# Kernel tuning notes

Hardware: AMD Instinct MI355X
Metric: run time of the kernel (lower is better)

Reference implementation:

```python
import jax, jax.numpy as jnp
import numpy as np
from jax import lax

VOL = 96 ** 3        # AvgPool3d(kernel_size=96) pooling volume
GAMMA = 0.2          # cam_threshold (gamma default in update())
NUM_CLASSES = 14


def conv3d_same(x, w, b):
    # Conv3d(kernel_size=3, padding=1), NCDHW layout
    y = lax.conv_general_dilated(
        x, w, window_strides=(1, 1, 1),
        padding=((1, 1), (1, 1), (1, 1)),
        dimension_numbers=('NCDHW', 'OIDHW', 'NCDHW'))
    return y + b[None, :, None, None, None]


def maxpool3d_2(x):
    return lax.reduce_window(x, -jnp.inf, lax.max,
                             (1, 1, 2, 2, 2), (1, 1, 2, 2, 2), 'VALID')


def dom_classifier(x, c1w, c1b, c2w, c2b, lw, lb):
    x = jax.nn.relu(maxpool3d_2(conv3d_same(x, c1w, c1b)))   # [N,128,2,2,2]
    x = jax.nn.relu(maxpool3d_2(conv3d_same(x, c2w, c2b)))   # [N,64,1,1,1]
    x = x.reshape(x.shape[0], -1)                            # [N,64]
    return x @ lw.T + lb                                     # [N,1]


def get_cam(feature):
    # torch.autograd.functional.jacobian of AvgPool3d(96) on a [1,C,96,96,96]
    # input is analytically delta(c,c')/96^3 at every voxel; the subsequent
    # mean over spatial dims keeps eye(C)/96^3. Same math, closed form.
    n, c = feature.shape[:2]
    weight = jnp.broadcast_to(jnp.eye(c, dtype=feature.dtype) / VOL, (n, c, c))
    # einsum(weight, feature, 'n cls ch, n ch h w d -> n cls h w d')
    cam = jnp.einsum('nkc,ncxyz->nkxyz', weight, feature)
    return jax.nn.relu(cam)


def reference(feature, masks, dom_feat, conv1_w, conv1_b, conv2_w, conv2_b,
              lin_w, lin_b):
    cam = get_cam(feature)[:, 1:]                 # drop background class
    cam = cam * (cam > GAMMA)                     # cam *= cam > threshold
    pseudo = jnp.argmax(cam, axis=1, keepdims=True).astype(masks.dtype)
    updated_masks = masks + pseudo * (masks == 0)
    dom_logits = dom_classifier(dom_feat, conv1_w, conv1_b,
                                conv2_w, conv2_b, lin_w, lin_b)
    return cam, pseudo, updated_masks, dom_logits


def setup_inputs() -> dict:
    key = jax.random.key(0)
    ks = jax.random.split(key, 8)
    return {
        'feature': jax.random.normal(ks[0], (2, NUM_CLASSES, 96, 96, 96), jnp.float32),
        'masks': jax.random.randint(ks[1], (2, 1, 96, 96, 96), 0, NUM_CLASSES, jnp.int32),
        'dom_feat': jax.random.normal(ks[2], (2, 256, 4, 4, 4), jnp.float32),
        'conv1_w': jax.random.normal(ks[3], (128, 256, 3, 3, 3), jnp.float32) * 0.05,
        'conv1_b': jnp.zeros((128,), jnp.float32),
        'conv2_w': jax.random.normal(ks[4], (64, 128, 3, 3, 3), jnp.float32) * 0.05,
        'conv2_b': jnp.zeros((64,), jnp.float32),
        'lin_w': jax.random.normal(ks[5], (1, 64), jnp.float32) * 0.05,
        'lin_b': jnp.zeros((1,), jnp.float32),
    }
```

## Files before the change

### kernel.cpp

```cpp
#include <hip/hip_runtime.h>

#define VOXELS   884736
#define OUT_CAM  0
#define OUT_PSE  23003136
#define OUT_MSK  24772608
#define OUT_LOG  26542080

#define WS_WT 0
#define WS_P  884736
#define WS_H1 1769472

typedef float  f32x4 __attribute__((ext_vector_type(4)));
typedef int    i32x4 __attribute__((ext_vector_type(4)));

#define THRESH(t)                                   \
  t.x = (t.x > 0.2f) ? t.x : 0.0f;                  \
  t.y = (t.y > 0.2f) ? t.y : 0.0f;                  \
  t.z = (t.z > 0.2f) ? t.z : 0.0f;                  \
  t.w = (t.w > 0.2f) ? t.w : 0.0f;

__global__ __launch_bounds__(256) void k_cam(const float* __restrict__ feat,
                                             const int*   __restrict__ masks,
                                             float* __restrict__ out) {
  int T = blockIdx.x * 256 + threadIdx.x;
  int n = T >= 110592;
  int v = (T - n * 110592) * 8;
  const float scale = 1.0f / 884736.0f;

  const float* fp = feat + (size_t)(n * 14 + 1) * VOXELS + v;
  const int*   mp = masks + (size_t)n * VOXELS + v;

  f32x4 fa[13], fb[13];
#pragma unroll
  for (int k = 0; k < 13; ++k) {
    fa[k] = *(const f32x4*)(fp + (size_t)k * VOXELS);
    fb[k] = *(const f32x4*)(fp + (size_t)k * VOXELS + 4);
  }
  i32x4 ma = *(const i32x4*)(mp);
  i32x4 mb = *(const i32x4*)(mp + 4);
  asm volatile("" : "+v"(fa[0]), "+v"(fa[1]), "+v"(fa[2]), "+v"(fa[3]),
                    "+v"(fa[4]), "+v"(fa[5]), "+v"(fa[6]), "+v"(fa[7]),
                    "+v"(fa[8]), "+v"(fa[9]), "+v"(fa[10]), "+v"(fa[11]),
                    "+v"(fa[12]));
  asm volatile("" : "+v"(fb[0]), "+v"(fb[1]), "+v"(fb[2]), "+v"(fb[3]),
                    "+v"(fb[4]), "+v"(fb[5]), "+v"(fb[6]), "+v"(fb[7]),
                    "+v"(fb[8]), "+v"(fb[9]), "+v"(fb[10]), "+v"(fb[11]),
                    "+v"(fb[12]));
  asm volatile("" : "+v"(ma), "+v"(mb));

#pragma unroll
  for (int k = 0; k < 13; ++k) {
    fa[k] *= scale; THRESH(fa[k]);
    fb[k] *= scale; THRESH(fb[k]);
  }

  float* cb = out + OUT_CAM + (size_t)(n * 13) * VOXELS + v;
#pragma unroll
  for (int k = 0; k < 13; ++k) {
    __builtin_nontemporal_store(fa[k], (f32x4*)(cb + (size_t)k * VOXELS));
    __builtin_nontemporal_store(fb[k], (f32x4*)(cb + (size_t)k * VOXELS + 4));
  }

  f32x4 best_a = fa[0], best_b = fb[0];
  i32x4 bia = {0, 0, 0, 0}, bib = {0, 0, 0, 0};
#pragma unroll
  for (int k = 1; k < 13; ++k) {
    if (fa[k].x > best_a.x) { best_a.x = fa[k].x; bia.x = k; }
    if (fa[k].y > best_a.y) { best_a.y = fa[k].y; bia.y = k; }
    if (fa[k].z > best_a.z) { best_a.z = fa[k].z; bia.z = k; }
    if (fa[k].w > best_a.w) { best_a.w = fa[k].w; bia.w = k; }
    if (fb[k].x > best_b.x) { best_b.x = fb[k].x; bib.x = k; }
    if (fb[k].y > best_b.y) { best_b.y = fb[k].y; bib.y = k; }
    if (fb[k].z > best_b.z) { best_b.z = fb[k].z; bib.z = k; }
    if (fb[k].w > best_b.w) { best_b.w = fb[k].w; bib.w = k; }
  }
  f32x4 psa = {(float)bia.x, (float)bia.y, (float)bia.z, (float)bia.w};
  f32x4 psb = {(float)bib.x, (float)bib.y, (float)bib.z, (float)bib.w};
  f32x4 uma, umb;
  uma.x = (ma.x == 0) ? psa.x : (float)ma.x;
  uma.y = (ma.y == 0) ? psa.y : (float)ma.y;
  uma.z = (ma.z == 0) ? psa.z : (float)ma.z;
  uma.w = (ma.w == 0) ? psa.w : (float)ma.w;
  umb.x = (mb.x == 0) ? psb.x : (float)mb.x;
  umb.y = (mb.y == 0) ? psb.y : (float)mb.y;
  umb.z = (mb.z == 0) ? psb.z : (float)mb.z;
  umb.w = (mb.w == 0) ? psb.w : (float)mb.w;
  float* pp = out + OUT_PSE + (size_t)n * VOXELS + v;
  float* up = out + OUT_MSK + (size_t)n * VOXELS + v;
  __builtin_nontemporal_store(psa, (f32x4*)pp);
  __builtin_nontemporal_store(psb, (f32x4*)(pp + 4));
  __builtin_nontemporal_store(uma, (f32x4*)up);
  __builtin_nontemporal_store(umb, (f32x4*)(up + 4));
}

__global__ __launch_bounds__(256) void k_trans(const float* __restrict__ w1,
                                               float* __restrict__ wt,
                                               float* __restrict__ logits) {
  __shared__ float s[6912];
  int r0 = blockIdx.x * 256;
  int tid = threadIdx.x;
  if (blockIdx.x == 0 && tid < 2) logits[tid] = 0.0f;
  for (int i = tid; i < 1728; i += 256)
    *(f32x4*)&s[i * 4] = *(const f32x4*)&w1[(size_t)r0 * 27 + i * 4];
  __syncthreads();
#pragma unroll
  for (int tap = 0; tap < 27; ++tap)
    wt[tap * 32768 + r0 + tid] = s[tid * 27 + tap];
}

#define WSTRIDE 68
__global__ __launch_bounds__(256) void k_conv1(const float* __restrict__ dom,
                                               const float* __restrict__ wt,
                                               float* __restrict__ P) {
  __shared__ float Wl[128 * WSTRIDE];
  __shared__ float Xl[128 * 64];
  int bx = blockIdx.x;
  int och = bx & 1;
  int ich = (bx >> 1) & 1;
  int rest = bx >> 2;
  int tap = rest % 27;
  int n = rest / 27;
  int kd = tap / 9 - 1, kh = (tap % 9) / 3 - 1, kw = tap % 3 - 1;
  int I0 = ich * 128, O0 = och * 64;
  int tid = threadIdx.x;

  for (int i = tid; i < 2048; i += 256) {
    int oc = i >> 5, k4 = (i & 31) << 2;
    f32x4 rd = *(const f32x4*)&wt[(size_t)(tap * 128 + O0 + oc) * 256 + I0 + k4];
    Wl[(k4 + 0) * WSTRIDE + oc] = rd.x;
    Wl[(k4 + 1) * WSTRIDE + oc] = rd.y;
    Wl[(k4 + 2) * WSTRIDE + oc] = rd.z;
    Wl[(k4 + 3) * WSTRIDE + oc] = rd.w;
  }
  for (int i = tid; i < 8192; i += 256) {
    int kk = i >> 6, pos = i & 63;
    int d = pos >> 4, h = (pos >> 2) & 3, w = pos & 3;
    int sd = d + kd, sh = h + kh, sw = w + kw;
    bool ok = ((unsigned)sd < 4u) && ((unsigned)sh < 4u) && ((unsigned)sw < 4u);
    Xl[i] = ok ? dom[((n * 256 + I0 + kk) << 6) + sd * 16 + sh * 4 + sw] : 0.0f;
  }
  __syncthreads();

  int to = tid >> 4, tp = tid & 15;
  f32x4 acc0 = {0, 0, 0, 0}, acc1 = {0, 0, 0, 0}, acc2 = {0, 0, 0, 0}, acc3 = {0, 0, 0, 0};
#pragma unroll 4
  for (int kk = 0; kk < 128; ++kk) {
    f32x4 a = *(f32x4*)&Wl[kk * WSTRIDE + to * 4];
    f32x4 b = *(f32x4*)&Xl[kk * 64 + tp * 4];
    acc0 += a.x * b;
    acc1 += a.y * b;
    acc2 += a.z * b;
    acc3 += a.w * b;
  }
  float* pb = P + (size_t)((tap * 2 + ich) * 2 + n) * 8192 + (O0 + to * 4) * 64 + tp * 4;
  *(f32x4*)(pb +   0) = acc0;
  *(f32x4*)(pb +  64) = acc1;
  *(f32x4*)(pb + 128) = acc2;
  *(f32x4*)(pb + 192) = acc3;
}

__global__ __launch_bounds__(256) void k_pool1(const float* __restrict__ P,
                                               const float* __restrict__ b1,
                                               float* __restrict__ h1) {
  __shared__ float s[256];
  int n = blockIdx.x >> 7, oc = blockIdx.x & 127;
  int tid = threadIdx.x, pos = tid & 63, sg = tid >> 6;
  float sum = 0.0f;
#pragma unroll
  for (int j = 0; j < 14; ++j) {
    int sl = sg + j * 4;
    if (sl < 54) sum += P[((size_t)(sl * 2 + n) * 128 + oc) * 64 + pos];
  }
  s[tid] = sum;
  __syncthreads();
  if (tid < 64) {
    float tot = b1[oc] + s[pos] + s[64 + pos] + s[128 + pos] + s[192 + pos];
    s[pos] = tot;
  }
  __syncthreads();
  if (tid < 8) {
    int pd = tid >> 2, ph = (tid >> 1) & 1, pw = tid & 1;
    float m = -3.402823466e38f;
#pragma unroll
    for (int dd = 0; dd < 2; ++dd)
#pragma unroll
      for (int hh = 0; hh < 2; ++hh)
#pragma unroll
        for (int ww = 0; ww < 2; ++ww)
          m = fmaxf(m, s[(pd * 2 + dd) * 16 + (ph * 2 + hh) * 4 + (pw * 2 + ww)]);
    h1[(n * 128 + oc) * 8 + tid] = fmaxf(m, 0.0f);
  }
}

__global__ __launch_bounds__(64) void k_conv2(const float* __restrict__ h1,
                                              const float* __restrict__ w2,
                                              const float* __restrict__ b2,
                                              const float* __restrict__ lw,
                                              const float* __restrict__ lb,
                                              float* __restrict__ logits) {
  __shared__ float hl[1024];
  __shared__ float wl[3456];
  __shared__ float red[64];
  int n = blockIdx.x >> 6, oc = blockIdx.x & 63;
  int tid = threadIdx.x;
  for (int i = tid; i < 1024; i += 64) hl[i] = h1[n * 1024 + i];
  for (int i = tid; i < 3456; i += 64) wl[i] = w2[oc * 3456 + i];
  __syncthreads();
  int p = tid & 7, g = tid >> 3;
  int d = p >> 2, h = (p >> 1) & 1, w = p & 1;
  float acc = 0.0f;
  for (int ic = g * 16; ic < g * 16 + 16; ++ic) {
#pragma unroll
    for (int a = 0; a < 2; ++a)
#pragma unroll
      for (int b = 0; b < 2; ++b)
#pragma unroll
        for (int c = 0; c < 2; ++c) {
          int tapi = (a - d + 1) * 9 + (b - h + 1) * 3 + (c - w + 1);
          acc += hl[ic * 8 + a * 4 + b * 2 + c] * wl[ic * 27 + tapi];
        }
  }
  red[tid] = acc;
  __syncthreads();
  if (tid == 0) {
    float mx = -3.402823466e38f;
#pragma unroll
    for (int pp = 0; pp < 8; ++pp) {
      float sv = b2[oc];
#pragma unroll
      for (int gg = 0; gg < 8; ++gg) sv += red[gg * 8 + pp];
      mx = fmaxf(mx, sv);
    }
    float h2v = fmaxf(mx, 0.0f);
    atomicAdd(&logits[n], h2v * lw[oc]);
    if (oc == 0) atomicAdd(&logits[n], lb[0]);
  }
}

extern "C" void kernel_launch(void* const* d_in, const int* in_sizes, int n_in,
                              void* d_out, int out_size, void* d_ws, size_t ws_size,
                              hipStream_t stream) {
  const float* feat  = (const float*)d_in[0];
  const int*   masks = (const int*)  d_in[1];
  const float* dom   = (const float*)d_in[2];
  const float* w1    = (const float*)d_in[3];
  const float* b1    = (const float*)d_in[4];
  const float* w2    = (const float*)d_in[5];
  const float* b2    = (const float*)d_in[6];
  const float* lw    = (const float*)d_in[7];
  const float* lb    = (const float*)d_in[8];
  float* out = (float*)d_out;
  float* ws  = (float*)d_ws;
  float* wt  = ws + WS_WT;
  float* P   = ws + WS_P;
  float* h1  = ws + WS_H1;
  float* logits = out + OUT_LOG;

  k_trans<<<128, 256, 0, stream>>>(w1, wt, logits);
  k_conv1<<<216, 256, 0, stream>>>(dom, wt, P);
  k_pool1<<<256, 256, 0, stream>>>(P, b1, h1);
  k_conv2<<<128, 64, 0, stream>>>(h1, w2, b2, lw, lb, logits);
  k_cam<<<864, 256, 0, stream>>>(feat, masks, out);
}
```

Before: 267.2 us.

## Split CAM kernel into elementwise threshold pass and argmax/mask pass

The fused CAM kernel is replaced by two kernels. The first is a fine-grained elementwise pass that scales, thresholds and writes the CAM with many small blocks. The second re-reads the written CAM to compute the argmax, pseudo labels and updated masks. The aim is more parallelism and memory-level concurrency than the register-heavy fused kernel allowed. The cost is an extra full read of the CAM output from memory and an additional launch, and the plain stores may leave the CAM in cache for reuse.

```diff
diff --git a/kernel.cpp b/kernel.cpp
--- a/kernel.cpp
+++ b/kernel.cpp
@@ -13,67 +13,46 @@
 typedef float  f32x4 __attribute__((ext_vector_type(4)));
 typedef int    i32x4 __attribute__((ext_vector_type(4)));
 
-#define THRESH(t)                                   \
-  t.x = (t.x > 0.2f) ? t.x : 0.0f;                  \
-  t.y = (t.y > 0.2f) ? t.y : 0.0f;                  \
-  t.z = (t.z > 0.2f) ? t.z : 0.0f;                  \
-  t.w = (t.w > 0.2f) ? t.w : 0.0f;
-
-__global__ __launch_bounds__(256) void k_cam(const float* __restrict__ feat,
-                                             const int*   __restrict__ masks,
-                                             float* __restrict__ out) {
+__global__ __launch_bounds__(256) void k_camA(const float* __restrict__ feat,
+                                              float* __restrict__ out) {
+  size_t i = ((size_t)blockIdx.x * 256 + threadIdx.x) * 4;
+  int n = i >= (size_t)13 * VOXELS;
+  const float scale = 1.0f / 884736.0f;
+  f32x4 f = *(const f32x4*)(feat + i + (size_t)(1 + n) * VOXELS);
+  f *= scale;
+  f.x = (f.x > 0.2f) ? f.x : 0.0f;
+  f.y = (f.y > 0.2f) ? f.y : 0.0f;
+  f.z = (f.z > 0.2f) ? f.z : 0.0f;
+  f.w = (f.w > 0.2f) ? f.w : 0.0f;
+  *(f32x4*)(out + OUT_CAM + i) = f;
+}
+
+__global__ __launch_bounds__(256) void k_camB(const int* __restrict__ masks,
+                                              float* out) {
   int T = blockIdx.x * 256 + threadIdx.x;
   int n = T >= 110592;
   int v = (T - n * 110592) * 8;
-  const float scale = 1.0f / 884736.0f;
-
-  const float* fp = feat + (size_t)(n * 14 + 1) * VOXELS + v;
-  const int*   mp = masks + (size_t)n * VOXELS + v;
-
-  f32x4 fa[13], fb[13];
-#pragma unroll
-  for (int k = 0; k < 13; ++k) {
-    fa[k] = *(const f32x4*)(fp + (size_t)k * VOXELS);
-    fb[k] = *(const f32x4*)(fp + (size_t)k * VOXELS + 4);
-  }
-  i32x4 ma = *(const i32x4*)(mp);
+  const float* cp = out + OUT_CAM + (size_t)(n * 13) * VOXELS + v;
+
+  f32x4 best_a = *(const f32x4*)cp;
+  f32x4 best_b = *(const f32x4*)(cp + 4);
+  i32x4 bia = {0, 0, 0, 0}, bib = {0, 0, 0, 0};
+#pragma unroll
+  for (int k = 1; k < 13; ++k) {
+    f32x4 ca = *(const f32x4*)(cp + (size_t)k * VOXELS);
+    f32x4 cb = *(const f32x4*)(cp + (size_t)k * VOXELS + 4);
+    if (ca.x > best_a.x) { best_a.x = ca.x; bia.x = k; }
+    if (ca.y > best_a.y) { best_a.y = ca.y; bia.y = k; }
+    if (ca.z > best_a.z) { best_a.z = ca.z; bia.z = k; }
+    if (ca.w > best_a.w) { best_a.w = ca.w; bia.w = k; }
+    if (cb.x > best_b.x) { best_b.x = cb.x; bib.x = k; }
+    if (cb.y > best_b.y) { best_b.y = cb.y; bib.y = k; }
+    if (cb.z > best_b.z) { best_b.z = cb.z; bib.z = k; }
+    if (cb.w > best_b.w) { best_b.w = cb.w; bib.w = k; }
+  }
+  const int* mp = masks + (size_t)n * VOXELS + v;
+  i32x4 ma = *(const i32x4*)mp;
   i32x4 mb = *(const i32x4*)(mp + 4);
-  asm volatile("" : "+v"(fa[0]), "+v"(fa[1]), "+v"(fa[2]), "+v"(fa[3]),
-                    "+v"(fa[4]), "+v"(fa[5]), "+v"(fa[6]), "+v"(fa[7]),
-                    "+v"(fa[8]), "+v"(fa[9]), "+v"(fa[10]), "+v"(fa[11]),
-                    "+v"(fa[12]));
-  asm volatile("" : "+v"(fb[0]), "+v"(fb[1]), "+v"(fb[2]), "+v"(fb[3]),
-                    "+v"(fb[4]), "+v"(fb[5]), "+v"(fb[6]), "+v"(fb[7]),
-                    "+v"(fb[8]), "+v"(fb[9]), "+v"(fb[10]), "+v"(fb[11]),
-                    "+v"(fb[12]));
-  asm volatile("" : "+v"(ma), "+v"(mb));
-
-#pragma unroll
-  for (int k = 0; k < 13; ++k) {
-    fa[k] *= scale; THRESH(fa[k]);
-    fb[k] *= scale; THRESH(fb[k]);
-  }
-
-  float* cb = out + OUT_CAM + (size_t)(n * 13) * VOXELS + v;
-#pragma unroll
-  for (int k = 0; k < 13; ++k) {
-    __builtin_nontemporal_store(fa[k], (f32x4*)(cb + (size_t)k * VOXELS));
-    __builtin_nontemporal_store(fb[k], (f32x4*)(cb + (size_t)k * VOXELS + 4));
-  }
-
-  f32x4 best_a = fa[0], best_b = fb[0];
-  i32x4 bia = {0, 0, 0, 0}, bib = {0, 0, 0, 0};
-#pragma unroll
-  for (int k = 1; k < 13; ++k) {
-    if (fa[k].x > best_a.x) { best_a.x = fa[k].x; bia.x = k; }
-    if (fa[k].y > best_a.y) { best_a.y = fa[k].y; bia.y = k; }
-    if (fa[k].z > best_a.z) { best_a.z = fa[k].z; bia.z = k; }
-    if (fa[k].w > best_a.w) { best_a.w = fa[k].w; bia.w = k; }
-    if (fb[k].x > best_b.x) { best_b.x = fb[k].x; bib.x = k; }
-    if (fb[k].y > best_b.y) { best_b.y = fb[k].y; bib.y = k; }
-    if (fb[k].z > best_b.z) { best_b.z = fb[k].z; bib.z = k; }
-    if (fb[k].w > best_b.w) { best_b.w = fb[k].w; bib.w = k; }
-  }
   f32x4 psa = {(float)bia.x, (float)bia.y, (float)bia.z, (float)bia.w};
   f32x4 psb = {(float)bib.x, (float)bib.y, (float)bib.z, (float)bib.w};
   f32x4 uma, umb;
@@ -260,5 +239,6 @@
   k_conv1<<<216, 256, 0, stream>>>(dom, wt, P);
   k_pool1<<<256, 256, 0, stream>>>(P, b1, h1);
   k_conv2<<<128, 64, 0, stream>>>(h1, w2, b2, lw, lb, logits);
-  k_cam<<<864, 256, 0, stream>>>(feat, masks, out);
-}
+  k_camA<<<22464, 256, 0, stream>>>(feat, out);
+  k_camB<<<864, 256, 0, stream>>>(masks, out);
+}
```

Result: faster. 248.0 us (-7.2%).
